# Optimization experiments

Measured on AMD Instinct MI355X. Metric: run time of the kernel, lower is better.

The kernel has to match this reference:

```python
import jax, jax.numpy as jnp
import numpy as np

N = 30000   # nodes
E = 240000  # edges
G = 16      # graphs in batch
DIMS = [1, 256, 512, 1024]
OUT = 1024

def _xavier(key, fan_in, fan_out):
    lim = float(np.sqrt(6.0 / (fan_in + fan_out)))
    return jax.random.uniform(key, (fan_in, fan_out), minval=-lim, maxval=lim, dtype=jnp.float32)

def setup_inputs() -> dict:
    key = jax.random.key(0)
    ks = jax.random.split(key, 8)
    x = jax.random.normal(ks[0], (N, DIMS[0]), dtype=jnp.float32)
    edge_index = jax.random.randint(ks[1], (2, E), 0, N, dtype=jnp.int64)
    batch = jnp.sort(jax.random.randint(ks[2], (N,), 0, G, dtype=jnp.int64))
    W1 = _xavier(ks[3], DIMS[0], DIMS[1]); b1 = jnp.zeros((DIMS[1],), jnp.float32)
    W2 = _xavier(ks[4], DIMS[1], DIMS[2]); b2 = jnp.zeros((DIMS[2],), jnp.float32)
    W3 = _xavier(ks[5], DIMS[2], DIMS[3]); b3 = jnp.zeros((DIMS[3],), jnp.float32)
    Wo = _xavier(ks[6], DIMS[3], OUT);     bo = jnp.zeros((OUT,), jnp.float32)
    return {"x": x, "edge_index": edge_index, "batch": batch,
            "W1": W1, "b1": b1, "W2": W2, "b2": b2, "W3": W3, "b3": b3,
            "Wo": Wo, "bo": bo}

def reference(x, edge_index, batch, W1, b1, W2, b2, W3, b3, Wo, bo):
    n = x.shape[0]
    loops = jnp.arange(n)
    # GCNConv adds self-loops, then symmetric deg^-1/2 normalization
    src = jnp.concatenate([edge_index[0], loops])
    dst = jnp.concatenate([edge_index[1], loops])
    deg = jnp.zeros((n,), jnp.float32).at[dst].add(1.0)  # >=1 due to self-loops
    dis = jax.lax.rsqrt(deg)
    norm = (dis[src] * dis[dst])[:, None]  # [E+N, 1]

    def gcn(h, W, b):
        h = h @ W                                   # linear (no bias in lin)
        agg = jnp.zeros_like(h).at[dst].add(h[src] * norm)  # scatter-add messages
        return agg + b                              # GCNConv bias

    h = jax.nn.relu(gcn(x, W1, b1))
    h = jax.nn.relu(gcn(h, W2, b2))
    h = jax.nn.relu(gcn(h, W3, b3))
    # global mean pool over graphs
    sums = jnp.zeros((G, h.shape[1]), h.dtype).at[batch].add(h)
    cnt = jnp.zeros((G,), h.dtype).at[batch].add(1.0)
    pooled = sums / jnp.maximum(cnt, 1.0)[:, None]
    return pooled @ Wo + bo
```

## Files before the change

### kernel.cpp

```cpp
#include <hip/hip_runtime.h>
#include <hip/hip_bf16.h>
#include <stdint.h>

#define N_NODES 30000
#define E_EDGES 240000
#define NGRAPH  16
#define D1      256
#define D2      512
#define D3      1024
#define DOUT    1024
#define M_PAD   30720
#define NT_M    240
#define CAP     40

typedef unsigned short ushort_t;
typedef short short8 __attribute__((ext_vector_type(8)));
typedef float f32x4 __attribute__((ext_vector_type(4)));

__device__ __forceinline__ float bf2f(ushort_t u) {
    union { unsigned int i; float f; } v; v.i = ((unsigned int)u) << 16; return v.f;
}
__device__ __forceinline__ ushort_t f2bf(float x) {
    union { float f; unsigned int i; } v; v.f = x;
    unsigned int r = v.i + 0x7fffu + ((v.i >> 16) & 1u);
    return (ushort_t)(r >> 16);
}

__device__ __forceinline__ int wave_isbf(const void* w1) {
    int lane = threadIdx.x & 63;
    float v = fabsf(bf2f(((const ushort_t*)w1)[lane * 2]));
    return __ballot(!(v <= 0.25f)) == 0ull;
}
__device__ __forceinline__ int wave_isi64(const void* ei) {
    int lane = threadIdx.x & 63;
    return __ballot(((const int*)ei)[lane * 2 + 1] != 0) == 0ull;
}

__global__ void k_setup(const void* x, const void* batch, const void* w1, const void* b1,
                        const void* b2, const void* b3, const void* bo,
                        const void* W2, const void* W3, const void* ei,
                        float* xf, int* batch32, float* W1f, float* b1f, float* b2f,
                        float* b3f, float* bof, ushort_t* Wt2, ushort_t* Wt3,
                        int* slotcnt, float* pooled, float* pooled2) {
    int isbf = wave_isbf(w1);
    int bid = blockIdx.x;
    int tid = threadIdx.x;
    if (bid < 492) {
        int i = bid * 256 + tid;
        if (i < 3072) {
            const void* src; float* dst; int idx;
            if      (i < 256)  { src = w1; dst = W1f; idx = i; }
            else if (i < 512)  { src = b1; dst = b1f; idx = i - 256; }
            else if (i < 1024) { src = b2; dst = b2f; idx = i - 512; }
            else if (i < 2048) { src = b3; dst = b3f; idx = i - 1024; }
            else               { src = bo; dst = bof; idx = i - 2048; }
            dst[idx] = isbf ? bf2f(((const ushort_t*)src)[idx]) : ((const float*)src)[idx];
        } else if (i < 33072) {
            int idx = i - 3072;
            xf[idx] = isbf ? bf2f(((const ushort_t*)x)[idx]) : ((const float*)x)[idx];
        } else if (i < 63072) {
            int idx = i - 33072;
            int isi64 = wave_isi64(ei);
            batch32[idx] = isi64 ? (int)((const long long*)batch)[idx]
                                 : ((const int*)batch)[idx];
        } else if (i < 93072) {
            slotcnt[i - 63072] = 0;
        } else if (i < 109456) {
            pooled[i - 93072] = 0.0f;
        } else if (i < 125840) {
            pooled2[i - 109456] = 0.0f;
        }
    } else {
        __shared__ ushort_t tile[32][33];
        int tb = bid - 492;
        const void* in; ushort_t* out; int R, C, bx, by;
        if (tb < 128) { in = W2; out = Wt2; R = D1; C = D2; bx = tb & 15; by = tb >> 4; }
        else { tb -= 128; in = W3; out = Wt3; R = D2; C = D3; bx = tb & 31; by = tb >> 5; }
        int tx = tid & 31, ty = tid >> 5;
        int c0 = bx * 32, r0 = by * 32;
        for (int i = ty; i < 32; i += 8) {
            size_t idx = (size_t)(r0 + i) * C + c0 + tx;
            tile[i][tx] = isbf ? ((const ushort_t*)in)[idx] : f2bf(((const float*)in)[idx]);
        }
        __syncthreads();
        for (int i = ty; i < 32; i += 8) out[(size_t)(c0 + i) * R + r0 + tx] = tile[tx][i];
    }
}

__global__ void k_edge_count(const void* ei, int* slotcnt, int* slots) {
    int isi64 = wave_isi64(ei);
    int e = blockIdx.x * 256 + threadIdx.x;
    if (e >= E_EDGES) return;
    int s, d;
    if (isi64) {
        s = (int)((const long long*)ei)[e];
        d = (int)((const long long*)ei)[E_EDGES + e];
    } else {
        s = ((const int*)ei)[e];
        d = ((const int*)ei)[E_EDGES + e];
    }
    if ((unsigned)s >= N_NODES || (unsigned)d >= N_NODES) return;
    int pos = atomicAdd(&slotcnt[d], 1);
    if (pos < CAP) slots[d * CAP + pos] = s;
}

__global__ void k_s1(const float* xf, const int* slotcnt, const int* slots,
                     const int* batch, float* dis, float* s1, float* cntg) {
    int b = blockIdx.x;
    if (b == 118) {
        int g = threadIdx.x;
        if (g >= NGRAPH) return;
        int lo0 = 0, hi0 = N_NODES;
        while (lo0 < hi0) { int m = (lo0 + hi0) >> 1; if (batch[m] < g) lo0 = m + 1; else hi0 = m; }
        int lo1 = lo0, hi1 = N_NODES;
        while (lo1 < hi1) { int m = (lo1 + hi1) >> 1; if (batch[m] < g + 1) lo1 = m + 1; else hi1 = m; }
        cntg[g] = (float)(lo1 - lo0);
        return;
    }
    int d = b * 256 + threadIdx.x;
    if (d >= N_NODES) return;
    int cd = slotcnt[d];
    float di = rsqrtf(1.0f + (float)cd);
    dis[d] = di;
    int cnt = cd < CAP ? cd : CAP;
    float acc = xf[d] * di;
    for (int k = 0; k < cnt; k++) {
        int s = slots[d * CAP + k];
        acc += xf[s] * rsqrtf(1.0f + (float)slotcnt[s]);
    }
    s1[d] = acc * di;
}

__global__ void k_agg1(const float* s1, const float* W1f, const float* b1f,
                       ushort_t* a2, const int* slots, const int* slotcnt, const float* dis) {
    int node = blockIdx.x * 4 + (threadIdx.x >> 6);
    int lane = threadIdx.x & 63;
    int c4 = lane * 4;
    float w[4], bb[4], a[4];
    #pragma unroll
    for (int j = 0; j < 4; j++) { w[j] = W1f[c4 + j]; bb[j] = b1f[c4 + j]; }
    float di = dis[node];
    int cnt = slotcnt[node]; cnt = cnt < CAP ? cnt : CAP;
    int s_l = (lane < cnt) ? slots[node * CAP + lane] : 0;
    float wn_l = dis[s_l] * di;
    float ss_l = s1[s_l];
    float sv = s1[node];
    float wsl = di * di;
    #pragma unroll
    for (int j = 0; j < 4; j++) a[j] = wsl * fmaxf(sv * w[j] + bb[j], 0.0f);
    for (int k = 0; k < cnt; k++) {
        float ss = __shfl(ss_l, k);
        float wn = __shfl(wn_l, k);
        #pragma unroll
        for (int j = 0; j < 4; j++) a[j] += wn * fmaxf(ss * w[j] + bb[j], 0.0f);
    }
    uint2 o;
    o.x = (unsigned int)f2bf(a[0]) | ((unsigned int)f2bf(a[1]) << 16);
    o.y = (unsigned int)f2bf(a[2]) | ((unsigned int)f2bf(a[3]) << 16);
    *(uint2*)&a2[(size_t)node * D1 + c4] = o;
}

__global__ void k_agg2(const ushort_t* h, ushort_t* out, const int* slots,
                       const int* slotcnt, const float* dis) {
    int node = blockIdx.x * 4 + (threadIdx.x >> 6);
    int lane = threadIdx.x & 63;
    int c8 = lane * 8;
    float di = dis[node];
    int cnt = slotcnt[node]; cnt = cnt < CAP ? cnt : CAP;
    int s_l = (lane < cnt) ? slots[node * CAP + lane] : 0;
    float ws_l = dis[s_l] * di;
    float w = di * di;
    const ushort_t* hp = h + c8;
    short8 p = *(const short8*)&hp[(size_t)node * D2];
    float a[8];
    #pragma unroll
    for (int j = 0; j < 8; j++) a[j] = w * bf2f((ushort_t)p[j]);
    if (cnt > 0) {
        int s0 = __shfl(s_l, 0);
        float ws0 = __shfl(ws_l, 0);
        short8 q0 = *(const short8*)&hp[(size_t)s0 * D2];
        for (int k = 1; k < cnt; k++) {
            int sk = __shfl(s_l, k);
            float ws1 = __shfl(ws_l, k);
            short8 q1 = *(const short8*)&hp[(size_t)sk * D2];
            #pragma unroll
            for (int j = 0; j < 8; j++) a[j] += ws0 * bf2f((ushort_t)q0[j]);
            q0 = q1; ws0 = ws1;
        }
        #pragma unroll
        for (int j = 0; j < 8; j++) a[j] += ws0 * bf2f((ushort_t)q0[j]);
    }
    uint4 o;
    o.x = (unsigned int)f2bf(a[0]) | ((unsigned int)f2bf(a[1]) << 16);
    o.y = (unsigned int)f2bf(a[2]) | ((unsigned int)f2bf(a[3]) << 16);
    o.z = (unsigned int)f2bf(a[4]) | ((unsigned int)f2bf(a[5]) << 16);
    o.w = (unsigned int)f2bf(a[6]) | ((unsigned int)f2bf(a[7]) << 16);
    *(uint4*)&out[(size_t)node * D2 + c8] = o;
}

#define GEMM_PROLOGUE_AND_LOOP(EPILOG_SYNC)                                            \
    uint4 ea0 = *(const uint4*)pA1, ea1 = *(const uint4*)pA2;                          \
    uint4 eb0 = *(const uint4*)pB1, eb1 = *(const uint4*)pB2;                          \
    *(uint4*)&As[0][off1] = ea0; *(uint4*)&As[0][off2] = ea1;                          \
    *(uint4*)&Bs[0][off1] = eb0; *(uint4*)&Bs[0][off2] = eb1;                          \
    uint4 oa0 = *(const uint4*)(pA1 + 32), oa1 = *(const uint4*)(pA2 + 32);            \
    uint4 ob0 = *(const uint4*)(pB1 + 32), ob1 = *(const uint4*)(pB2 + 32);            \
    asm volatile("s_waitcnt lgkmcnt(0)" ::: "memory");                                 \
    __builtin_amdgcn_s_barrier();                                                      \
    int rsw = (quad ^ ((l15 >> 1) & 3)) << 3;                                          \
    f32x4 acc[4][4];                                                                   \
    for (int a = 0; a < 4; a++)                                                        \
        for (int b = 0; b < 4; b++)                                                    \
            acc[a][b] = (f32x4){0.f, 0.f, 0.f, 0.f};                                   \
    int niter = K >> 5;                                                                \
    for (int t = 0; t < niter; t += 2) {                                               \
                        \
        int k2 = (t + 2) << 5;                                                         \
        if (k2 < K) {                                                                  \
            ea0 = *(const uint4*)(pA1 + k2); ea1 = *(const uint4*)(pA2 + k2);          \
            eb0 = *(const uint4*)(pB1 + k2); eb1 = *(const uint4*)(pB2 + k2);          \
        }                                                                              \
        {                                                                              \
            short8 af[4], bfr[4];                                                      \
            for (int im = 0; im < 4; im++)                                             \
                af[im] = *(const short8*)&As[0][(wm + im * 16 + l15) * 32 + rsw];      \
            for (int in = 0; in < 4; in++)                                             \
                bfr[in] = *(const short8*)&Bs[0][(wn + in * 16 + l15) * 32 + rsw];     \
            for (int im = 0; im < 4; im++)                                             \
                for (int in = 0; in < 4; in++)                                         \
                    acc[im][in] = __builtin_amdgcn_mfma_f32_16x16x32_bf16(af[im], bfr[in], acc[im][in], 0, 0, 0); \
        }                                                                              \
        *(uint4*)&As[1][off1] = oa0; *(uint4*)&As[1][off2] = oa1;                      \
        *(uint4*)&Bs[1][off1] = ob0; *(uint4*)&Bs[1][off2] = ob1;                      \
        asm volatile("s_waitcnt lgkmcnt(0)" ::: "memory");                             \
        __builtin_amdgcn_s_barrier();                                                  \
                       \
        int k3 = (t + 3) << 5;                                                         \
        if (k3 < K) {                                                                  \
            oa0 = *(const uint4*)(pA1 + k3); oa1 = *(const uint4*)(pA2 + k3);          \
            ob0 = *(const uint4*)(pB1 + k3); ob1 = *(const uint4*)(pB2 + k3);          \
        }                                                                              \
        {                                                                              \
            short8 af[4], bfr[4];                                                      \
            for (int im = 0; im < 4; im++)                                             \
                af[im] = *(const short8*)&As[1][(wm + im * 16 + l15) * 32 + rsw];      \
            for (int in = 0; in < 4; in++)                                             \
                bfr[in] = *(const short8*)&Bs[1][(wn + in * 16 + l15) * 32 + rsw];     \
            for (int im = 0; im < 4; im++)                                             \
                for (int in = 0; in < 4; in++)                                         \
                    acc[im][in] = __builtin_amdgcn_mfma_f32_16x16x32_bf16(af[im], bfr[in], acc[im][in], 0, 0, 0); \
        }                                                                              \
        if (k2 < K) {                                                                  \
            *(uint4*)&As[0][off1] = ea0; *(uint4*)&As[0][off2] = ea1;                  \
            *(uint4*)&Bs[0][off1] = eb0; *(uint4*)&Bs[0][off2] = eb1;                  \
        }                                                                              \
        asm volatile("s_waitcnt lgkmcnt(0)" ::: "memory");                             \
        __builtin_amdgcn_s_barrier();                                                  \
    }                                                                                  \
    EPILOG_SYNC

__global__ __launch_bounds__(256, 3) void k_gemm(const ushort_t* A, const ushort_t* Bt,
                                                 const float* bias, ushort_t* Cmat,
                                                 int K, int Ncols, int ntn) {
    __shared__ __align__(16) ushort_t As[2][128 * 32];
    __shared__ __align__(16) ushort_t Bs[2][128 * 32];
    int tid = threadIdx.x;
    int id = blockIdx.x;
    int xcd = id & 7, q = id >> 3;
    int rt = xcd * (NT_M / 8) + q / ntn;
    int ct = q % ntn;
    int bm0 = rt * 128, bn0 = ct * 128;
    int wave = tid >> 6, lane = tid & 63;
    int wm = (wave & 1) * 64, wn = (wave >> 1) * 64;
    int l15 = lane & 15, quad = lane >> 4;

    int m1 = tid >> 2, kc = tid & 3, k1 = kc << 3;
    int wsw = (kc ^ ((m1 >> 1) & 3)) << 3;
    int off1 = m1 * 32 + wsw, off2 = off1 + 64 * 32;
    const ushort_t* pA1 = A + (size_t)(bm0 + m1) * K + k1;
    const ushort_t* pA2 = pA1 + (size_t)64 * K;
    const ushort_t* pB1 = Bt + (size_t)(bn0 + m1) * K + k1;
    const ushort_t* pB2 = pB1 + (size_t)64 * K;

    GEMM_PROLOGUE_AND_LOOP()

    for (int im = 0; im < 4; im++) {
        int row = bm0 + wm + im * 16 + quad * 4;
        for (int in = 0; in < 4; in++) {
            int col = bn0 + wn + in * 16 + l15;
            float bv = bias[col];
            for (int r = 0; r < 4; r++) {
                float v = acc[im][in][r] + bv;
                v = v > 0.0f ? v : 0.0f;
                Cmat[(size_t)(row + r) * Ncols + col] = f2bf(v);
            }
        }
    }
}

__global__ __launch_bounds__(256, 3) void k_gemm_pool(const ushort_t* A, const ushort_t* Bt,
                                                      const float* bias, const int* batch,
                                                      float* pooled, int K, int ntn) {
    __shared__ __align__(16) ushort_t As[2][128 * 32];
    __shared__ __align__(16) ushort_t Bs[2][128 * 32];
    int tid = threadIdx.x;
    int id = blockIdx.x;
    int xcd = id & 7, q = id >> 3;
    int rt = xcd * (NT_M / 8) + q / ntn;
    int ct = q % ntn;
    int bm0 = rt * 128, bn0 = ct * 128;
    int wave = tid >> 6, lane = tid & 63;
    int wm = (wave & 1) * 64, wn = (wave >> 1) * 64;
    int l15 = lane & 15, quad = lane >> 4;

    int m1 = tid >> 2, kc = tid & 3, k1 = kc << 3;
    int wsw = (kc ^ ((m1 >> 1) & 3)) << 3;
    int off1 = m1 * 32 + wsw, off2 = off1 + 64 * 32;
    const ushort_t* pA1 = A + (size_t)(bm0 + m1) * K + k1;
    const ushort_t* pA2 = pA1 + (size_t)64 * K;
    const ushort_t* pB1 = Bt + (size_t)(bn0 + m1) * K + k1;
    const ushort_t* pB2 = pB1 + (size_t)64 * K;

    GEMM_PROLOGUE_AND_LOOP(__syncthreads();)

    float* pl = (float*)&As[0][0];
    int* gtile = (int*)&Bs[0][0];
    for (int i = tid; i < NGRAPH * 128; i += 256) pl[i] = 0.0f;
    if (tid < 128) {
        int r = bm0 + tid; if (r > N_NODES - 1) r = N_NODES - 1;
        int g = batch[r]; g = g < 0 ? 0 : (g > NGRAPH - 1 ? NGRAPH - 1 : g);
        gtile[tid] = g;
    }
    __syncthreads();

    int gmin = gtile[0], gmax = gtile[127];
    if (gmin == gmax && bm0 + 127 < N_NODES) {
        float csum[4];
        #pragma unroll
        for (int in = 0; in < 4; in++) csum[in] = 0.0f;
        for (int im = 0; im < 4; im++) {
            #pragma unroll
            for (int in = 0; in < 4; in++) {
                float bv = bias[bn0 + wn + in * 16 + l15];
                #pragma unroll
                for (int r = 0; r < 4; r++)
                    csum[in] += fmaxf(acc[im][in][r] + bv, 0.0f);
            }
        }
        #pragma unroll
        for (int in = 0; in < 4; in++) {
            csum[in] += __shfl_xor(csum[in], 16);
            csum[in] += __shfl_xor(csum[in], 32);
        }
        if (quad == 0) {
            #pragma unroll
            for (int in = 0; in < 4; in++)
                atomicAdd(&pl[gmin * 128 + wn + in * 16 + l15], csum[in]);
        }
    } else {
        for (int im = 0; im < 4; im++) {
            int rl = wm + im * 16 + quad * 4;
            for (int in = 0; in < 4; in++) {
                int cl = wn + in * 16 + l15;
                float bv = bias[bn0 + cl];
                float vsum = 0.0f;
                int gprev = gtile[rl];
                for (int r = 0; r < 4; r++) {
                    int row = bm0 + rl + r;
                    float v = (row < N_NODES) ? fmaxf(acc[im][in][r] + bv, 0.0f) : 0.0f;
                    int g = gtile[rl + r];
                    if (g != gprev) {
                        atomicAdd(&pl[gprev * 128 + cl], vsum);
                        vsum = 0.0f; gprev = g;
                    }
                    vsum += v;
                }
                atomicAdd(&pl[gprev * 128 + cl], vsum);
            }
        }
    }
    __syncthreads();

    int span = (gmax - gmin + 1) * 128;
    for (int idx = tid; idx < span; idx += 256) {
        int g = gmin + (idx >> 7), cl = idx & 127;
        float v = pl[g * 128 + cl];
        if (v != 0.0f) atomicAdd(&pooled[g * DOUT + bn0 + cl], v);
    }
}

__global__ __launch_bounds__(256) void k_out_partial(const float* pooled, const void* Wo,
                                                     float* pooled2, const void* w1) {
    __shared__ float pl[NGRAPH * 32];
    int tid = threadIdx.x;
    int col = blockIdx.x * 256 + tid;
    int k0 = blockIdx.y * 32;
    for (int i = tid; i < NGRAPH * 32; i += 256) {
        int g = i >> 5, kk = i & 31;
        pl[i] = pooled[g * D3 + k0 + kk];
    }
    __syncthreads();
    int isbf = wave_isbf(w1);
    float acc[NGRAPH];
    #pragma unroll
    for (int g = 0; g < NGRAPH; g++) acc[g] = 0.0f;
    #pragma unroll 4
    for (int kk = 0; kk < 32; kk++) {
        int k = k0 + kk;
        float wv = isbf ? bf2f(((const ushort_t*)Wo)[(size_t)k * DOUT + col])
                        : ((const float*)Wo)[(size_t)k * DOUT + col];
        #pragma unroll
        for (int g = 0; g < NGRAPH; g++)
            acc[g] += pl[g * 32 + kk] * wv;
    }
    #pragma unroll
    for (int g = 0; g < NGRAPH; g++)
        atomicAdd(&pooled2[g * DOUT + col], acc[g]);
}

__global__ void k_out_fin(const float* pooled2, const float* bof, const float* cntg,
                          void* out, const void* w1) {
    int isbf = wave_isbf(w1);
    int i = blockIdx.x * 256 + threadIdx.x;
    int g = i >> 10, o = i & 1023;
    float c = cntg[g]; c = c > 1.0f ? c : 1.0f;
    float v = pooled2[i] / c + bof[o];
    if (isbf) ((ushort_t*)out)[i] = f2bf(v);
    else      ((float*)out)[i] = v;
}

extern "C" void kernel_launch(void* const* d_in, const int* in_sizes, int n_in,
                              void* d_out, int out_size, void* d_ws, size_t ws_size,
                              hipStream_t stream) {
    const void* x_raw  = d_in[0];
    const void* ei_raw = d_in[1];
    const void* b_raw  = d_in[2];
    const void* W1_raw = d_in[3];
    const void* b1_raw = d_in[4];
    const void* W2_raw = d_in[5];
    const void* b2_raw = d_in[6];
    const void* W3_raw = d_in[7];
    const void* b3_raw = d_in[8];
    const void* Wo_raw = d_in[9];
    const void* bo_raw = d_in[10];

    char* w = (char*)d_ws;
    size_t off = 0;
    auto alloc = [&](size_t b) { size_t o = off; off += (b + 255) & ~(size_t)255; return o; };
    float* xf      = (float*)(w + alloc((size_t)N_NODES * 4));
    int*   batch32 = (int*)  (w + alloc((size_t)N_NODES * 4));
    float* W1f     = (float*)(w + alloc(D1 * 4));
    float* b1f     = (float*)(w + alloc(D1 * 4));
    float* b2f     = (float*)(w + alloc(D2 * 4));
    float* b3f     = (float*)(w + alloc(D3 * 4));
    float* bof     = (float*)(w + alloc(DOUT * 4));
    float* dis     = (float*)(w + alloc((size_t)N_NODES * 4));
    float* s1      = (float*)(w + alloc((size_t)N_NODES * 4));
    float* cntg    = (float*)(w + alloc(64));
    float* pooled  = (float*)(w + alloc((size_t)NGRAPH * DOUT * 4));
    float* pooled2 = (float*)(w + alloc((size_t)NGRAPH * DOUT * 4));
    int*   slotcnt = (int*)  (w + alloc((size_t)N_NODES * 4));
    int*   slots   = (int*)  (w + alloc((size_t)N_NODES * CAP * 4));
    ushort_t* Wt2  = (ushort_t*)(w + alloc((size_t)D2 * D1 * 2));
    ushort_t* Wt3  = (ushort_t*)(w + alloc((size_t)D3 * D2 * 2));
    ushort_t* slabA = (ushort_t*)(w + alloc((size_t)M_PAD * D2 * 2));
    ushort_t* a2 = slabA;
    ushort_t* a3 = slabA;
    ushort_t* h2   = (ushort_t*)(w + alloc((size_t)M_PAD * D2 * 2));

    int nb_e = (E_EDGES + 255) / 256;

    k_setup<<<1132, 256, 0, stream>>>(x_raw, b_raw, W1_raw, b1_raw, b2_raw, b3_raw, bo_raw,
                                      W2_raw, W3_raw, ei_raw, xf, batch32, W1f, b1f, b2f,
                                      b3f, bof, Wt2, Wt3, slotcnt, pooled, pooled2);
    k_edge_count<<<nb_e, 256, 0, stream>>>(ei_raw, slotcnt, slots);
    k_s1<<<119, 256, 0, stream>>>(xf, slotcnt, slots, batch32, dis, s1, cntg);

    k_agg1<<<N_NODES / 4, 256, 0, stream>>>(s1, W1f, b1f, a2, slots, slotcnt, dis);
    k_gemm<<<NT_M * (D2 / 128), 256, 0, stream>>>(a2, Wt2, b2f, h2, D1, D2, D2 / 128);
    k_agg2<<<N_NODES / 4, 256, 0, stream>>>(h2, a3, slots, slotcnt, dis);
    k_gemm_pool<<<NT_M * (D3 / 128), 256, 0, stream>>>(a3, Wt3, b3f, batch32, pooled, D2, D3 / 128);

    k_out_partial<<<dim3(DOUT / 256, D3 / 32), 256, 0, stream>>>(pooled, Wo_raw, pooled2, W1_raw);
    k_out_fin<<<NGRAPH * DOUT / 256, 256, 0, stream>>>(pooled2, bof, cntg, d_out, W1_raw);
}
```

Measured before the change: 232.5 us.

## Merge setup with edge bucketing, fuse output projection and finalize

The setup kernel and the edge-bucketing kernel are merged into one launch, and zeroing of the counters and pooled buffer moves to hipMemsetAsync. The output projection now has each 64-thread block compute complete dot products over K, split in two halves and combined with a shuffle, then apply the mean divide and bias directly. This removes the atomic partial accumulation, the separate finalize kernel and the per-graph count pass. The tradeoff is that edge bucketing now runs concurrently with setup in the same grid, and the output kernel recomputes the graph counts by binary search in every block. Each thread also reads Wo with a column stride over 512 rows.

```diff
diff --git a/kernel.cpp b/kernel.cpp
--- a/kernel.cpp
+++ b/kernel.cpp
@@ -36,16 +36,16 @@
     return __ballot(((const int*)ei)[lane * 2 + 1] != 0) == 0ull;
 }
 
-__global__ void k_setup(const void* x, const void* batch, const void* w1, const void* b1,
-                        const void* b2, const void* b3, const void* bo,
-                        const void* W2, const void* W3, const void* ei,
-                        float* xf, int* batch32, float* W1f, float* b1f, float* b2f,
-                        float* b3f, float* bof, ushort_t* Wt2, ushort_t* Wt3,
-                        int* slotcnt, float* pooled, float* pooled2) {
-    int isbf = wave_isbf(w1);
+__global__ void k_setup_edge(const void* x, const void* batch, const void* w1, const void* b1,
+                             const void* b2, const void* b3, const void* bo,
+                             const void* W2, const void* W3, const void* ei,
+                             float* xf, int* batch32, float* W1f, float* b1f, float* b2f,
+                             float* b3f, float* bof, ushort_t* Wt2, ushort_t* Wt3,
+                             int* slotcnt, int* slots) {
     int bid = blockIdx.x;
     int tid = threadIdx.x;
-    if (bid < 492) {
+    if (bid < 247) {
+        int isbf = wave_isbf(w1);
         int i = bid * 256 + tid;
         if (i < 3072) {
             const void* src; float* dst; int idx;
@@ -63,16 +63,11 @@
             int isi64 = wave_isi64(ei);
             batch32[idx] = isi64 ? (int)((const long long*)batch)[idx]
                                  : ((const int*)batch)[idx];
-        } else if (i < 93072) {
-            slotcnt[i - 63072] = 0;
-        } else if (i < 109456) {
-            pooled[i - 93072] = 0.0f;
-        } else if (i < 125840) {
-            pooled2[i - 109456] = 0.0f;
-        }
-    } else {
+        }
+    } else if (bid < 887) {
+        int isbf = wave_isbf(w1);
         __shared__ ushort_t tile[32][33];
-        int tb = bid - 492;
+        int tb = bid - 247;
         const void* in; ushort_t* out; int R, C, bx, by;
         if (tb < 128) { in = W2; out = Wt2; R = D1; C = D2; bx = tb & 15; by = tb >> 4; }
         else { tb -= 128; in = W3; out = Wt3; R = D2; C = D3; bx = tb & 31; by = tb >> 5; }
@@ -84,40 +79,27 @@
         }
         __syncthreads();
         for (int i = ty; i < 32; i += 8) out[(size_t)(c0 + i) * R + r0 + tx] = tile[tx][i];
-    }
-}
-
-__global__ void k_edge_count(const void* ei, int* slotcnt, int* slots) {
-    int isi64 = wave_isi64(ei);
-    int e = blockIdx.x * 256 + threadIdx.x;
-    if (e >= E_EDGES) return;
-    int s, d;
-    if (isi64) {
-        s = (int)((const long long*)ei)[e];
-        d = (int)((const long long*)ei)[E_EDGES + e];
     } else {
-        s = ((const int*)ei)[e];
-        d = ((const int*)ei)[E_EDGES + e];
-    }
-    if ((unsigned)s >= N_NODES || (unsigned)d >= N_NODES) return;
-    int pos = atomicAdd(&slotcnt[d], 1);
-    if (pos < CAP) slots[d * CAP + pos] = s;
+        int isi64 = wave_isi64(ei);
+        int e = (bid - 887) * 256 + tid;
+        if (e >= E_EDGES) return;
+        int s, d;
+        if (isi64) {
+            s = (int)((const long long*)ei)[e];
+            d = (int)((const long long*)ei)[E_EDGES + e];
+        } else {
+            s = ((const int*)ei)[e];
+            d = ((const int*)ei)[E_EDGES + e];
+        }
+        if ((unsigned)s >= N_NODES || (unsigned)d >= N_NODES) return;
+        int pos = atomicAdd(&slotcnt[d], 1);
+        if (pos < CAP) slots[d * CAP + pos] = s;
+    }
 }
 
 __global__ void k_s1(const float* xf, const int* slotcnt, const int* slots,
-                     const int* batch, float* dis, float* s1, float* cntg) {
-    int b = blockIdx.x;
-    if (b == 118) {
-        int g = threadIdx.x;
-        if (g >= NGRAPH) return;
-        int lo0 = 0, hi0 = N_NODES;
-        while (lo0 < hi0) { int m = (lo0 + hi0) >> 1; if (batch[m] < g) lo0 = m + 1; else hi0 = m; }
-        int lo1 = lo0, hi1 = N_NODES;
-        while (lo1 < hi1) { int m = (lo1 + hi1) >> 1; if (batch[m] < g + 1) lo1 = m + 1; else hi1 = m; }
-        cntg[g] = (float)(lo1 - lo0);
-        return;
-    }
-    int d = b * 256 + threadIdx.x;
+                     float* dis, float* s1) {
+    int d = blockIdx.x * 256 + threadIdx.x;
     if (d >= N_NODES) return;
     int cd = slotcnt[d];
     float di = rsqrtf(1.0f + (float)cd);
@@ -214,7 +196,6 @@
             acc[a][b] = (f32x4){0.f, 0.f, 0.f, 0.f};                                   \
     int niter = K >> 5;                                                                \
     for (int t = 0; t < niter; t += 2) {                                               \
-                        \
         int k2 = (t + 2) << 5;                                                         \
         if (k2 < K) {                                                                  \
             ea0 = *(const uint4*)(pA1 + k2); ea1 = *(const uint4*)(pA2 + k2);          \
@@ -234,7 +215,6 @@
         *(uint4*)&Bs[1][off1] = ob0; *(uint4*)&Bs[1][off2] = ob1;                      \
         asm volatile("s_waitcnt lgkmcnt(0)" ::: "memory");                             \
         __builtin_amdgcn_s_barrier();                                                  \
-                       \
         int k3 = (t + 3) << 5;                                                         \
         if (k3 < K) {                                                                  \
             oa0 = *(const uint4*)(pA1 + k3); oa1 = *(const uint4*)(pA2 + k3);          \
@@ -389,44 +369,48 @@
     }
 }
 
-__global__ __launch_bounds__(256) void k_out_partial(const float* pooled, const void* Wo,
-                                                     float* pooled2, const void* w1) {
-    __shared__ float pl[NGRAPH * 32];
-    int tid = threadIdx.x;
-    int col = blockIdx.x * 256 + tid;
-    int k0 = blockIdx.y * 32;
-    for (int i = tid; i < NGRAPH * 32; i += 256) {
-        int g = i >> 5, kk = i & 31;
-        pl[i] = pooled[g * D3 + k0 + kk];
-    }
-    __syncthreads();
+__global__ __launch_bounds__(64) void k_out(const float* pooled, const void* Wo,
+                                            const float* bof, const int* batch,
+                                            void* out, const void* w1) {
     int isbf = wave_isbf(w1);
-    float acc[NGRAPH];
-    #pragma unroll
-    for (int g = 0; g < NGRAPH; g++) acc[g] = 0.0f;
-    #pragma unroll 4
-    for (int kk = 0; kk < 32; kk++) {
-        int k = k0 + kk;
-        float wv = isbf ? bf2f(((const ushort_t*)Wo)[(size_t)k * DOUT + col])
-                        : ((const float*)Wo)[(size_t)k * DOUT + col];
-        #pragma unroll
-        for (int g = 0; g < NGRAPH; g++)
-            acc[g] += pl[g * 32 + kk] * wv;
-    }
-    #pragma unroll
-    for (int g = 0; g < NGRAPH; g++)
-        atomicAdd(&pooled2[g * DOUT + col], acc[g]);
-}
-
-__global__ void k_out_fin(const float* pooled2, const float* bof, const float* cntg,
-                          void* out, const void* w1) {
-    int isbf = wave_isbf(w1);
-    int i = blockIdx.x * 256 + threadIdx.x;
-    int g = i >> 10, o = i & 1023;
-    float c = cntg[g]; c = c > 1.0f ? c : 1.0f;
-    float v = pooled2[i] / c + bof[o];
-    if (isbf) ((ushort_t*)out)[i] = f2bf(v);
-    else      ((float*)out)[i] = v;
+    int lane = threadIdx.x & 63;
+    int half = lane >> 5;
+    int idx = blockIdx.x * 32 + (lane & 31);
+    int g = idx >> 10, col = idx & 1023;
+    int kbase = half * (D3 / 2);
+    float a0 = 0.f, a1 = 0.f, a2 = 0.f, a3 = 0.f;
+    const float* pg = pooled + g * D3;
+    if (isbf) {
+        const ushort_t* wo = (const ushort_t*)Wo;
+        #pragma unroll 4
+        for (int k = kbase; k < kbase + D3 / 2; k += 4) {
+            a0 += pg[k]     * bf2f(wo[(size_t)k * DOUT + col]);
+            a1 += pg[k + 1] * bf2f(wo[(size_t)(k + 1) * DOUT + col]);
+            a2 += pg[k + 2] * bf2f(wo[(size_t)(k + 2) * DOUT + col]);
+            a3 += pg[k + 3] * bf2f(wo[(size_t)(k + 3) * DOUT + col]);
+        }
+    } else {
+        const float* wo = (const float*)Wo;
+        #pragma unroll 4
+        for (int k = kbase; k < kbase + D3 / 2; k += 4) {
+            a0 += pg[k]     * wo[(size_t)k * DOUT + col];
+            a1 += pg[k + 1] * wo[(size_t)(k + 1) * DOUT + col];
+            a2 += pg[k + 2] * wo[(size_t)(k + 2) * DOUT + col];
+            a3 += pg[k + 3] * wo[(size_t)(k + 3) * DOUT + col];
+        }
+    }
+    float acc = (a0 + a1) + (a2 + a3);
+    acc += __shfl_xor(acc, 32);
+    if (half == 0) {
+        int lo0 = 0, hi0 = N_NODES;
+        while (lo0 < hi0) { int m = (lo0 + hi0) >> 1; if (batch[m] < g) lo0 = m + 1; else hi0 = m; }
+        int lo1 = lo0, hi1 = N_NODES;
+        while (lo1 < hi1) { int m = (lo1 + hi1) >> 1; if (batch[m] < g + 1) lo1 = m + 1; else hi1 = m; }
+        float c = (float)(lo1 - lo0); c = c > 1.0f ? c : 1.0f;
+        float v = acc / c + bof[col];
+        if (isbf) ((ushort_t*)out)[idx] = f2bf(v);
+        else      ((float*)out)[idx] = v;
+    }
 }
 
 extern "C" void kernel_launch(void* const* d_in, const int* in_sizes, int n_in,
@@ -456,9 +440,7 @@
     float* bof     = (float*)(w + alloc(DOUT * 4));
     float* dis     = (float*)(w + alloc((size_t)N_NODES * 4));
     float* s1      = (float*)(w + alloc((size_t)N_NODES * 4));
-    float* cntg    = (float*)(w + alloc(64));
     float* pooled  = (float*)(w + alloc((size_t)NGRAPH * DOUT * 4));
-    float* pooled2 = (float*)(w + alloc((size_t)NGRAPH * DOUT * 4));
     int*   slotcnt = (int*)  (w + alloc((size_t)N_NODES * 4));
     int*   slots   = (int*)  (w + alloc((size_t)N_NODES * CAP * 4));
     ushort_t* Wt2  = (ushort_t*)(w + alloc((size_t)D2 * D1 * 2));
@@ -468,19 +450,19 @@
     ushort_t* a3 = slabA;
     ushort_t* h2   = (ushort_t*)(w + alloc((size_t)M_PAD * D2 * 2));
 
-    int nb_e = (E_EDGES + 255) / 256;
-
-    k_setup<<<1132, 256, 0, stream>>>(x_raw, b_raw, W1_raw, b1_raw, b2_raw, b3_raw, bo_raw,
-                                      W2_raw, W3_raw, ei_raw, xf, batch32, W1f, b1f, b2f,
-                                      b3f, bof, Wt2, Wt3, slotcnt, pooled, pooled2);
-    k_edge_count<<<nb_e, 256, 0, stream>>>(ei_raw, slotcnt, slots);
-    k_s1<<<119, 256, 0, stream>>>(xf, slotcnt, slots, batch32, dis, s1, cntg);
+    hipMemsetAsync(slotcnt, 0, (size_t)N_NODES * 4, stream);
+    hipMemsetAsync(pooled, 0, (size_t)NGRAPH * DOUT * 4, stream);
+
+    k_setup_edge<<<1825, 256, 0, stream>>>(x_raw, b_raw, W1_raw, b1_raw, b2_raw, b3_raw,
+                                           bo_raw, W2_raw, W3_raw, ei_raw, xf, batch32,
+                                           W1f, b1f, b2f, b3f, bof, Wt2, Wt3,
+                                           slotcnt, slots);
+    k_s1<<<118, 256, 0, stream>>>(xf, slotcnt, slots, dis, s1);
 
     k_agg1<<<N_NODES / 4, 256, 0, stream>>>(s1, W1f, b1f, a2, slots, slotcnt, dis);
     k_gemm<<<NT_M * (D2 / 128), 256, 0, stream>>>(a2, Wt2, b2f, h2, D1, D2, D2 / 128);
     k_agg2<<<N_NODES / 4, 256, 0, stream>>>(h2, a3, slots, slotcnt, dis);
     k_gemm_pool<<<NT_M * (D3 / 128), 256, 0, stream>>>(a3, Wt3, b3f, batch32, pooled, D2, D3 / 128);
 
-    k_out_partial<<<dim3(DOUT / 256, D3 / 32), 256, 0, stream>>>(pooled, Wo_raw, pooled2, W1_raw);
-    k_out_fin<<<NGRAPH * DOUT / 256, 256, 0, stream>>>(pooled2, bof, cntg, d_out, W1_raw);
-}
+    k_out<<<NGRAPH * DOUT / 32, 64, 0, stream>>>(pooled, Wo_raw, bof, batch32, d_out, W1_raw);
+}
```

Result: slower. 254.5 us (+9.4%).
